# Kernel tuning notes

Measured on AMD Instinct MI355X. Metric: run time of the kernel, lower is better.

Reference implementation:

```python
import jax, jax.numpy as jnp
import numpy as np

H = 200   # hidden_size
P = 4     # maxout_pool_size
T = 4     # max_dec_steps
B = 64
M = 1000
NEG = -1e30


def setup_inputs():
    key = jax.random.key(0)
    ks = jax.random.split(key, 20)
    def rn(k, shape, scale=0.05):
        return jax.random.normal(k, shape, dtype=jnp.float32) * scale
    inp = {}
    inp["U"] = jax.random.normal(ks[0], (B, M, 2 * H), dtype=jnp.float32)
    inp["d_mask"] = jnp.ones((B, M), dtype=jnp.int32)
    inp["span"] = jax.random.randint(ks[1], (B, 2), 0, M)
    # LSTM: input 4H, hidden H, 1 layer, torch forget-gate bias init (f gate = 1)
    inp["w_ih"] = rn(ks[2], (4 * H, 4 * H))
    inp["w_hh"] = rn(ks[3], (4 * H, H))
    inp["b_ih"] = jnp.zeros((4 * H,), jnp.float32).at[H:2 * H].set(1.0)
    inp["b_hh"] = jnp.zeros((4 * H,), jnp.float32)
    # two HighwayMaxout heads (start 's', end 'e')
    for tag, off in (("s", 4), ("e", 11)):
        inp[f"Wr_{tag}"] = rn(ks[off + 0], (H, 5 * H))          # linear, no bias
        inp[f"W1_{tag}"] = rn(ks[off + 1], (H * P, 3 * H))
        inp[f"b1_{tag}"] = jnp.zeros((H * P,), jnp.float32)
        inp[f"W2_{tag}"] = rn(ks[off + 2], (H * P, H))
        inp[f"b2_{tag}"] = jnp.zeros((H * P,), jnp.float32)
        inp[f"W12_{tag}"] = rn(ks[off + 3], (P, 2 * H))
        inp[f"b12_{tag}"] = jnp.zeros((P,), jnp.float32)
    return inp


def lstm_step(x, h, c, w_ih, w_hh, b_ih, b_hh):
    # torch gate order: i, f, g, o
    g = x @ w_ih.T + h @ w_hh.T + b_ih + b_hh
    i, f, gg, o = jnp.split(g, 4, axis=-1)
    c = jax.nn.sigmoid(f) * c + jax.nn.sigmoid(i) * jnp.tanh(gg)
    h = jax.nn.sigmoid(o) * jnp.tanh(c)
    return h, c


def hmn(h, U, u_cat, mask_mult, Wr, W1, b1, W2, b2, W12, b12):
    b, m, _ = U.shape
    r = jnp.tanh(jnp.concatenate([h, u_cat], 1) @ Wr.T)                      # (b,H)
    x = jnp.concatenate([U, jnp.broadcast_to(r[:, None, :], (b, m, H))], 2)  # (b,m,3H)
    m1 = (x @ W1.T + b1).reshape(b, m, H, P).max(-1)                          # (b,m,H)
    m2 = (m1 @ W2.T + b2).reshape(b, m, H, P).max(-1)                         # (b,m,H)
    alpha = (jnp.concatenate([m1, m2], 2) @ W12.T + b12).max(-1)             # (b,m)
    return jax.nn.log_softmax(alpha + mask_mult, axis=1)


def reference(U, d_mask, span, w_ih, w_hh, b_ih, b_hh,
              Wr_s, W1_s, b1_s, W2_s, b2_s, W12_s, b12_s,
              Wr_e, W1_e, b1_e, W2_e, b2_e, W12_e, b12_e):
    b, m, _ = U.shape
    bidx = jnp.arange(b)
    mask_mult = (1.0 - d_mask.astype(jnp.float32)) * NEG
    s_tgt = span[:, 0]
    e_tgt = span[:, 1]
    ps = (Wr_s, W1_s, b1_s, W2_s, b2_s, W12_s, b12_s)
    pe = (Wr_e, W1_e, b1_e, W2_e, b2_e, W12_e, b12_e)

    s0 = jnp.zeros((b,), jnp.int32)
    e0 = (jnp.sum(d_mask, 1) - 1).astype(jnp.int32)
    u_s0 = U[bidx, s0]
    h0 = jnp.zeros((b, H), U.dtype)
    c0 = jnp.zeros((b, H), U.dtype)
    m0 = jnp.ones((b,), bool)

    def step(carry, first):
        s, e, u_s, h, c, ms, me = carry
        u_e = U[bidx, e]
        u_cat = jnp.concatenate([u_s, u_e], 1)               # (b,4H)
        h, c = lstm_step(u_cat, h, c, w_ih, w_hh, b_ih, b_hh)
        # start head
        a_s = hmn(h, U, u_cat, mask_mult, *ps)
        idx_s = jnp.argmax(a_s, 1).astype(jnp.int32)
        s_new = jnp.where(first, idx_s, idx_s * ms)
        ms_new = jnp.where(first, True, s_new != s * ms)
        ls = -jnp.mean(jnp.take_along_axis(a_s, s_tgt[:, None], 1)) * ms_new.astype(U.dtype)
        # end head (u_s refreshed with new start)
        u_s2 = U[bidx, s_new]
        u_cat2 = jnp.concatenate([u_s2, u_e], 1)
        a_e = hmn(h, U, u_cat2, mask_mult, *pe)
        idx_e = jnp.argmax(a_e, 1).astype(jnp.int32)
        e_new = jnp.where(first, idx_e, idx_e * me)
        me_new = jnp.where(first, True, e_new != e * me)
        le = -jnp.mean(jnp.take_along_axis(a_e, e_tgt[:, None], 1)) * me_new.astype(U.dtype)
        return (s_new, e_new, u_s2, h, c, ms_new, me_new), (s_new, ms_new, e_new, me_new, ls + le)

    firsts = jnp.arange(T) == 0
    _, (ss, mss, es, mes, losses) = jax.lax.scan(step, (s0, e0, u_s0, h0, c0, m0, m0), firsts)

    pos_s = jnp.sum(mss.astype(jnp.int32), 0) - 1            # (b,)
    p1 = ss[pos_s, bidx]
    pos_e = jnp.sum(mes.astype(jnp.int32), 0) - 1
    p2 = es[pos_e, bidx]
    loss = jnp.mean(jnp.sum(losses, 0)) / T
    return loss, p1, p2
```

## Files before the change

kernel.cpp:

```cpp
#include <hip/hip_runtime.h>
#include <math.h>

#define H 200
#define TT 4
#define BB 64
#define MM 1000
#define NEGV (-1e30f)

static const int ROWS = BB * MM;
#define KA 416
#define KB 224
#define NPAD 896
#define NSLICE 28
#define LSTR 40
#define RP 500
#define GG 3528

typedef __attribute__((ext_vector_type(8))) short short8;
typedef __attribute__((ext_vector_type(4))) float f32x4;

__device__ __forceinline__ void split2(float x, unsigned short& h, unsigned short& l) {
  unsigned u = __float_as_uint(x);
  h = (unsigned short)(u >> 16);
  float res = x - __uint_as_float(u & 0xffff0000u);
  l = (unsigned short)(__float_as_uint(res) >> 16);
}
__device__ __forceinline__ float bf2f(unsigned short h) {
  return __uint_as_float(((unsigned)h) << 16);
}
__device__ __forceinline__ void gload16(const unsigned short* g, const unsigned short* l) {
  __builtin_amdgcn_global_load_lds(
      (const __attribute__((address_space(1))) void*)g,
      (__attribute__((address_space(3))) void*)l, 16, 0, 0);
}

__global__ __launch_bounds__(256) void k_init(const int* __restrict__ dmask,
    int* st_s, int* st_e, int* ms, int* me,
    float* h, float* c, float* out) {
  int b = blockIdx.x, t = threadIdx.x;
  __shared__ int red[256];
  int sum = 0;
  for (int m = t; m < MM; m += 256) sum += dmask[b * MM + m];
  red[t] = sum; __syncthreads();
  for (int s = 128; s > 0; s >>= 1) { if (t < s) red[t] += red[t + s]; __syncthreads(); }
  if (t == 0) { st_s[b] = 0; st_e[b] = red[0] - 1; ms[b] = 1; me[b] = 1; }
  for (int i = t; i < H; i += 256) { h[b * H + i] = 0.f; c[b * H + i] = 0.f; }
  if (b == 0 && t == 0) out[0] = 0.f;
}

__global__ __launch_bounds__(256) void k_splitP(const float* __restrict__ src, int srcld,
    int Ksrc, int Nsrc,
    unsigned short* __restrict__ hi, unsigned short* __restrict__ lo, int Kpad) {
  int r = blockIdx.x;
  int r7 = r & 127;
  size_t pbase = (size_t)(r >> 7) * (size_t)(128 * Kpad);
  int sw = (r7 >> 1) & 3;
  for (int k = threadIdx.x; k < Kpad; k += 256) {
    unsigned short h = 0, l = 0;
    if (r < Nsrc && k < Ksrc) split2(src[(size_t)r * srcld + k], h, l);
    size_t addr = pbase + (size_t)(k >> 5) * 4096 + r7 * 32 +
                  ((((k >> 3) & 3) ^ sw) << 3) + (k & 7);
    hi[addr] = h; lo[addr] = l;
  }
}

__global__ __launch_bounds__(256) void k_splitPW1(const float* __restrict__ src,
    unsigned short* __restrict__ hi, unsigned short* __restrict__ lo) {
  int r = blockIdx.x;
  int o = (r & ~63) + ((r & 15) << 2) + ((r >> 4) & 3);
  int r7 = r & 127;
  size_t pbase = (size_t)(r >> 7) * (size_t)(128 * KA);
  int sw = (r7 >> 1) & 3;
  for (int k = threadIdx.x; k < KA; k += 256) {
    unsigned short h = 0, l = 0;
    if (o < 800 && k < 400) split2(src[(size_t)o * 600 + k], h, l);
    size_t addr = pbase + (size_t)(k >> 5) * 4096 + r7 * 32 +
                  ((((k >> 3) & 3) ^ sw) << 3) + (k & 7);
    hi[addr] = h; lo[addr] = l;
  }
}

__global__ __launch_bounds__(256) void k_split(const float* __restrict__ src, int srcld,
    int Ksrc, int Nsrc,
    unsigned short* __restrict__ hi, unsigned short* __restrict__ lo, int Kpad) {
  int r = blockIdx.x;
  for (int k = threadIdx.x; k < Kpad; k += 256) {
    unsigned short h = 0, l = 0;
    if (r < Nsrc && k < Ksrc) split2(src[(size_t)r * srcld + k], h, l);
    hi[(size_t)r * Kpad + k] = h;
    lo[(size_t)r * Kpad + k] = l;
  }
}

__global__ __launch_bounds__(1024) void k_lstm_r(
    const float* __restrict__ U, const int* __restrict__ st_s, const int* __restrict__ st_e,
    float* __restrict__ h, float* __restrict__ c,
    const float* __restrict__ w_ih, const float* __restrict__ w_hh,
    const float* __restrict__ b_ih, const float* __restrict__ b_hh,
    const float* __restrict__ Wr, const float* __restrict__ W1, const float* __restrict__ b1,
    float* __restrict__ rcorr, float* __restrict__ ue) {
  int b = blockIdx.x, t = threadIdx.x;
  __shared__ float xc[1000];
  __shared__ float hold[H];
  __shared__ float g[800];
  __shared__ float r[H];
  int si = st_s[b], ei = st_e[b];
  const float* Us = U + ((size_t)b * MM + si) * 400;
  const float* Ue = U + ((size_t)b * MM + ei) * 400;
  if (t < 400) { xc[200 + t] = Us[t]; xc[600 + t] = Ue[t]; ue[b * 400 + t] = Ue[t]; }
  if (t >= 400 && t < 600) hold[t - 400] = h[b * H + (t - 400)];
  __syncthreads();
  if (t < 800) {
    float acc = b_ih[t] + b_hh[t];
    const float4* wi = (const float4*)(w_ih + (size_t)t * 800);
    const float* xv = &xc[200];
    for (int k = 0; k < 200; ++k) {
      float4 wv = wi[k];
      acc = fmaf(wv.x, xv[k * 4 + 0], acc); acc = fmaf(wv.y, xv[k * 4 + 1], acc);
      acc = fmaf(wv.z, xv[k * 4 + 2], acc); acc = fmaf(wv.w, xv[k * 4 + 3], acc);
    }
    const float4* wh = (const float4*)(w_hh + (size_t)t * H);
    for (int k = 0; k < 50; ++k) {
      float4 wv = wh[k];
      acc = fmaf(wv.x, hold[k * 4 + 0], acc); acc = fmaf(wv.y, hold[k * 4 + 1], acc);
      acc = fmaf(wv.z, hold[k * 4 + 2], acc); acc = fmaf(wv.w, hold[k * 4 + 3], acc);
    }
    g[t] = acc;
  }
  __syncthreads();
  if (t < H) {
    float ig = 1.f / (1.f + expf(-g[t]));
    float fg = 1.f / (1.f + expf(-g[H + t]));
    float gg = tanhf(g[2 * H + t]);
    float og = 1.f / (1.f + expf(-g[3 * H + t]));
    float cn = fg * c[b * H + t] + ig * gg;
    c[b * H + t] = cn;
    float hv = og * tanhf(cn);
    h[b * H + t] = hv;
    xc[t] = hv;
  }
  __syncthreads();
  if (t < H) {
    float acc = 0.f;
    const float4* wr = (const float4*)(Wr + (size_t)t * 1000);
    for (int k = 0; k < 250; ++k) {
      float4 wv = wr[k];
      acc = fmaf(wv.x, xc[k * 4 + 0], acc); acc = fmaf(wv.y, xc[k * 4 + 1], acc);
      acc = fmaf(wv.z, xc[k * 4 + 2], acc); acc = fmaf(wv.w, xc[k * 4 + 3], acc);
    }
    r[t] = tanhf(acc);
  }
  __syncthreads();
  if (t < NPAD) {
    float acc = 0.f;
    if (t < 800) {
      acc = b1[t];
      const float4* w1 = (const float4*)(W1 + (size_t)t * 600 + 400);
      for (int k = 0; k < 50; ++k) {
        float4 wv = w1[k];
        acc = fmaf(wv.x, r[k * 4 + 0], acc); acc = fmaf(wv.y, r[k * 4 + 1], acc);
        acc = fmaf(wv.z, r[k * 4 + 2], acc); acc = fmaf(wv.w, r[k * 4 + 3], acc);
      }
    }
    rcorr[b * NPAD + t] = acc;
  }
}

__global__ __launch_bounds__(1024) void k_re(
    const float* __restrict__ U, const int* __restrict__ st_s,
    const float* __restrict__ ue, const float* __restrict__ h,
    const float* __restrict__ Wr, const float* __restrict__ W1, const float* __restrict__ b1,
    float* __restrict__ rcorr) {
  int b = blockIdx.x, t = threadIdx.x;
  __shared__ float xc[1000];
  __shared__ float r[H];
  const float* Us = U + ((size_t)b * MM + st_s[b]) * 400;
  if (t < 200) xc[t] = h[b * H + t];
  if (t >= 200 && t < 600) xc[t] = Us[t - 200];
  if (t >= 600 && t < 1000) xc[t] = ue[b * 400 + (t - 600)];
  __syncthreads();
  if (t < H) {
    float acc = 0.f;
    const float4* wr = (const float4*)(Wr + (size_t)t * 1000);
    for (int k = 0; k < 250; ++k) {
      float4 wv = wr[k];
      acc = fmaf(wv.x, xc[k * 4 + 0], acc); acc = fmaf(wv.y, xc[k * 4 + 1], acc);
      acc = fmaf(wv.z, xc[k * 4 + 2], acc); acc = fmaf(wv.w, xc[k * 4 + 3], acc);
    }
    r[t] = tanhf(acc);
  }
  __syncthreads();
  if (t < NPAD) {
    float acc = 0.f;
    if (t < 800) {
      acc = b1[t];
      const float4* w1 = (const float4*)(W1 + (size_t)t * 600 + 400);
      for (int k = 0; k < 50; ++k) {
        float4 wv = w1[k];
        acc = fmaf(wv.x, r[k * 4 + 0], acc); acc = fmaf(wv.y, r[k * 4 + 1], acc);
        acc = fmaf(wv.z, r[k * 4 + 2], acc); acc = fmaf(wv.w, r[k * 4 + 3], acc);
      }
    }
    rcorr[b * NPAD + t] = acc;
  }
}

template <int MODE>
__global__ __launch_bounds__(256, 3) void k_pgemm(
    const unsigned short* __restrict__ Ah, const unsigned short* __restrict__ Al,
    const unsigned short* __restrict__ Bh, const unsigned short* __restrict__ Bl,
    const float* __restrict__ addv,
    unsigned short* __restrict__ Couth, unsigned short* __restrict__ Coutl,
    float* __restrict__ partial, const float* __restrict__ W12) {
  const int Kpad = (MODE == 0) ? KA : KB;
  const int nk = Kpad >> 5;
  __shared__ unsigned short sA[2][8192];
  __shared__ unsigned short sB[8192];
  const int id = blockIdx.x;
  const int g = id / 56, rem = id % 56;
  const int np = rem >> 3, c8 = rem & 7;
  const int rp = g * 8 + c8;
  if (rp >= RP) return;
  const int tid = threadIdx.x;
  const int lane = tid & 63, wave = tid >> 6;
  const int wm = wave >> 1, wn = wave & 1;
  const int row0 = rp * 128, n0 = np * 128;
  const int lr = lane & 15, ls = lane >> 4;
  const size_t panelA = (size_t)rp * (size_t)(128 * Kpad);
  const size_t panelB = (size_t)np * (size_t)(128 * Kpad);
  const int aoff = (wm * 64 + lr) * 32 + ((ls ^ ((lr >> 1) & 3)) << 3);
  const int boff = (wn * 64 + lr) * 32 + ((ls ^ ((lr >> 1) & 3)) << 3);

  f32x4 acc[4][4];
#pragma unroll
  for (int i = 0; i < 4; ++i)
#pragma unroll
    for (int j = 0; j < 4; ++j) acc[i][j] = (f32x4){0.f, 0.f, 0.f, 0.f};

  auto issueA = [&](int buf, int kt) {
    const size_t tA = panelA + (size_t)kt * 4096;
#pragma unroll
    for (int q = 0; q < 2; ++q) {
      const int cc = (q * 4 + wave) * 512;
      gload16(Ah + tA + cc + lane * 8, &sA[buf][cc]);
      gload16(Al + tA + cc + lane * 8, &sA[buf][4096 + cc]);
    }
  };
  auto issueB = [&](int kt) {
    const size_t tB = panelB + (size_t)kt * 4096;
#pragma unroll
    for (int q = 0; q < 2; ++q) {
      const int cc = (q * 4 + wave) * 512;
      gload16(Bh + tB + cc + lane * 8, &sB[cc]);
      gload16(Bl + tB + cc + lane * 8, &sB[4096 + cc]);
    }
  };

  issueA(0, 0);
  issueB(0);
  int cur = 0;
  for (int kt = 0; kt < nk; ++kt) {
    __syncthreads();
    short8 bh[4], bl[4], fah[4], fal[4];
#pragma unroll
    for (int j = 0; j < 4; ++j) {
      bh[j] = *(const short8*)(sB + boff + j * 512);
      bl[j] = *(const short8*)(sB + 4096 + boff + j * 512);
    }
#pragma unroll
    for (int i = 0; i < 4; ++i) {
      fah[i] = *(const short8*)(&sA[cur][0] + aoff + i * 512);
      fal[i] = *(const short8*)(&sA[cur][0] + 4096 + aoff + i * 512);
    }
    __syncthreads();
    if (kt + 1 < nk) { issueA(cur ^ 1, kt + 1); issueB(kt + 1); }
#pragma unroll
    for (int i = 0; i < 4; ++i)
#pragma unroll
      for (int j = 0; j < 4; ++j)
        acc[i][j] = __builtin_amdgcn_mfma_f32_16x16x32_bf16(fah[i], bh[j], acc[i][j], 0, 0, 0);
#pragma unroll
    for (int i = 0; i < 4; ++i)
#pragma unroll
      for (int j = 0; j < 4; ++j)
        acc[i][j] = __builtin_amdgcn_mfma_f32_16x16x32_bf16(fah[i], bl[j], acc[i][j], 0, 0, 0);
#pragma unroll
    for (int i = 0; i < 4; ++i)
#pragma unroll
      for (int j = 0; j < 4; ++j)
        acc[i][j] = __builtin_amdgcn_mfma_f32_16x16x32_bf16(fal[i], bh[j], acc[i][j], 0, 0, 0);
    cur ^= 1;
  }

  if (MODE == 0) {
    const int obase = n0 + wn * 64 + lr * 4;
    const int po = ((n0 + wn * 64) >> 2) + lr;
    const unsigned b0 = (unsigned)row0 / 1000u;
    const unsigned b1 = (unsigned)(row0 + 127) / 1000u;
    float rc0[4], rc1[4];
#pragma unroll
    for (int j = 0; j < 4; ++j) {
      rc0[j] = addv[b0 * NPAD + obase + j];
      rc1[j] = addv[b1 * NPAD + obase + j];
    }
    const size_t panelC = (size_t)rp * (size_t)(128 * KB);
    const size_t addrBase = panelC + (size_t)(po >> 5) * 4096 + (po & 7);
    const int slotb = (po >> 3) & 3;
    const int rowb7 = wm * 64 + ls * 4;
#pragma unroll
    for (int i = 0; i < 4; ++i) {
#pragma unroll
      for (int r = 0; r < 4; ++r) {
        const int r7 = rowb7 + i * 16 + r;
        const int row = row0 + r7;
        const bool useb0 = ((unsigned)row / 1000u) == b0;
        float v = acc[i][0][r] + (useb0 ? rc0[0] : rc1[0]);
        v = fmaxf(v, acc[i][1][r] + (useb0 ? rc0[1] : rc1[1]));
        v = fmaxf(v, acc[i][2][r] + (useb0 ? rc0[2] : rc1[2]));
        v = fmaxf(v, acc[i][3][r] + (useb0 ? rc0[3] : rc1[3]));
        const int sw = (r7 >> 1) & 3;
        size_t addr = addrBase + r7 * 32 + ((slotb ^ sw) << 3);
        unsigned short hh, ll;
        split2(v, hh, ll);
        Couth[addr] = hh;
        Coutl[addr] = ll;
      }
    }
  } else {
    const int colb = n0 + wn * 64 + lr;
    const int rowb7 = wm * 64 + ls * 4;
    const int pmine = lane & 3;
    float w12j[4], addj[4];
#pragma unroll
    for (int j = 0; j < 4; ++j) {
      const int col = colb + j * 16;
      w12j[j] = (col < 800) ? W12[pmine * 400 + 200 + (col >> 2)] : 0.f;
      addj[j] = (col < 800) ? addv[col] : 0.f;
    }
    const int slice = np * 2 + wn;
#pragma unroll
    for (int i = 0; i < 4; ++i) {
#pragma unroll
      for (int r = 0; r < 4; ++r) {
        const int row = row0 + rowb7 + i * 16 + r;
        float sp = 0.f;
#pragma unroll
        for (int j = 0; j < 4; ++j) {
          float v = acc[i][j][r] + addj[j];
          v = fmaxf(v, __shfl_xor(v, 1));
          v = fmaxf(v, __shfl_xor(v, 2));
          sp = fmaf(v, w12j[j], sp);
        }
        sp += __shfl_xor(sp, 4);
        sp += __shfl_xor(sp, 8);
        if (lr < 4)
          partial[((size_t)row * 14 + slice) * 4 + lr] = sp;
      }
    }
  }
}

__global__ __launch_bounds__(256) void k_m1dot(
    const unsigned short* __restrict__ m1h, const unsigned short* __restrict__ m1l,
    const float* __restrict__ partial, const float* __restrict__ W12,
    const float* __restrict__ b12, float* __restrict__ alpha) {
  __shared__ float w12s[4 * 224];
  __shared__ unsigned short th[4096], tl[4096];
  __shared__ float accs[128 * 8];
  const int t = threadIdx.x;
  const int rp = blockIdx.x;
  for (int i = t; i < 896; i += 256) {
    int p = i / 224, k = i - p * 224;
    w12s[i] = (k < 200) ? W12[p * 400 + k] : 0.f;
  }
  const int r7 = t & 127, hhalf = t >> 7;
  const int sw = (r7 >> 1) & 3;
  float a0 = 0.f, a1 = 0.f, a2 = 0.f, a3 = 0.f;
  const size_t panelC = (size_t)rp * (size_t)(128 * KB);
  for (int kt = 0; kt < 7; ++kt) {
    __syncthreads();
    const size_t tb = panelC + (size_t)kt * 4096;
    *(short8*)&th[t * 16] = *(const short8*)(m1h + tb + t * 16);
    *(short8*)&th[t * 16 + 8] = *(const short8*)(m1h + tb + t * 16 + 8);
    *(short8*)&tl[t * 16] = *(const short8*)(m1l + tb + t * 16);
    *(short8*)&tl[t * 16 + 8] = *(const short8*)(m1l + tb + t * 16 + 8);
    __syncthreads();
#pragma unroll
    for (int cc = 0; cc < 2; ++cc) {
      const int c = hhalf * 2 + cc;
      const short8 hv = *(const short8*)&th[r7 * 32 + ((c ^ sw) << 3)];
      const short8 lv = *(const short8*)&tl[r7 * 32 + ((c ^ sw) << 3)];
      const int kb = kt * 32 + c * 8;
#pragma unroll
      for (int e = 0; e < 8; ++e) {
        float val = bf2f((unsigned short)hv[e]) + bf2f((unsigned short)lv[e]);
        const int k = kb + e;
        a0 = fmaf(val, w12s[0 * 224 + k], a0);
        a1 = fmaf(val, w12s[1 * 224 + k], a1);
        a2 = fmaf(val, w12s[2 * 224 + k], a2);
        a3 = fmaf(val, w12s[3 * 224 + k], a3);
      }
    }
  }
  accs[r7 * 8 + hhalf * 4 + 0] = a0;
  accs[r7 * 8 + hhalf * 4 + 1] = a1;
  accs[r7 * 8 + hhalf * 4 + 2] = a2;
  accs[r7 * 8 + hhalf * 4 + 3] = a3;
  __syncthreads();
  if (t < 128) {
    const size_t row = (size_t)rp * 128 + t;
    float4 bb = *(const float4*)b12;
    float s0 = bb.x + accs[t * 8 + 0] + accs[t * 8 + 4];
    float s1 = bb.y + accs[t * 8 + 1] + accs[t * 8 + 5];
    float s2 = bb.z + accs[t * 8 + 2] + accs[t * 8 + 6];
    float s3 = bb.w + accs[t * 8 + 3] + accs[t * 8 + 7];
    const float4* pr = (const float4*)(partial + row * 56);
#pragma unroll
    for (int s = 0; s < 14; ++s) {
      float4 p4 = pr[s];
      s0 += p4.x; s1 += p4.y; s2 += p4.z; s3 += p4.w;
    }
    alpha[row] = fmaxf(fmaxf(s0, s1), fmaxf(s2, s3));
  }
}

__global__ __launch_bounds__(256) void k_argmax(const float* __restrict__ alpha,
    const int* __restrict__ dmask, const int* __restrict__ span, int tag,
    int* __restrict__ idx_out, float* __restrict__ atgt_out) {
  int b = blockIdx.x, t = threadIdx.x;
  __shared__ float vals[MM];
  __shared__ float rv[256];
  __shared__ int ri[256];
  float bestv = -3.4e38f; int besti = 0x7fffffff;
  for (int m = t; m < MM; m += 256) {
    float v = alpha[b * MM + m];
    if (!dmask[b * MM + m]) v += NEGV;
    vals[m] = v;
    if (v > bestv || (v == bestv && m < besti)) { bestv = v; besti = m; }
  }
  rv[t] = bestv; ri[t] = besti; __syncthreads();
  for (int s = 128; s > 0; s >>= 1) {
    if (t < s) {
      float v2 = rv[t + s]; int i2 = ri[t + s];
      if (v2 > rv[t] || (v2 == rv[t] && i2 < ri[t])) { rv[t] = v2; ri[t] = i2; }
    }
    __syncthreads();
  }
  float vmax = rv[0]; int vidx = ri[0];
  __syncthreads();
  float se = 0.f;
  for (int m = t; m < MM; m += 256) se += expf(vals[m] - vmax);
  rv[t] = se; __syncthreads();
  for (int s = 128; s > 0; s >>= 1) { if (t < s) rv[t] += rv[t + s]; __syncthreads(); }
  if (t == 0) {
    int tgt = span[b * 2 + tag];
    atgt_out[b] = vals[tgt] - vmax - logf(rv[0]);
    idx_out[b] = vidx;
  }
}

template <int MODE, int PRESPLIT>
__global__ __launch_bounds__(256) void k_mgemm(
    const float* __restrict__ Af, int lda, int KsrcA,
    const unsigned short* __restrict__ Ah, const unsigned short* __restrict__ Al,
    const unsigned short* __restrict__ Bh, const unsigned short* __restrict__ Bl, int Kpad,
    const float* __restrict__ addv,
    unsigned short* __restrict__ Couth, unsigned short* __restrict__ Coutl,
    float* __restrict__ partial, const float* __restrict__ W12, int slice_base) {
  __shared__ unsigned short sAh[128 * LSTR], sAl[128 * LSTR];
  __shared__ unsigned short sBh[128 * LSTR], sBl[128 * LSTR];
  const int tid = threadIdx.x;
  const int lane = tid & 63, wave = tid >> 6;
  const int wm = wave >> 1, wn = wave & 1;
  const int n0 = blockIdx.x * 128, row0 = blockIdx.y * 128;
  const int lr = lane & 15, ls = lane >> 4;
  f32x4 acc[4][4];
#pragma unroll
  for (int i = 0; i < 4; ++i)
#pragma unroll
    for (int j = 0; j < 4; ++j) acc[i][j] = (f32x4){0.f, 0.f, 0.f, 0.f};
  const int srow = tid >> 1, shalf = tid & 1;
  const float* Afp = Af ? (Af + (size_t)(row0 + srow) * lda + shalf * 16) : nullptr;
  const unsigned short* Ahp = Ah ? (Ah + (size_t)(row0 + srow) * Kpad + shalf * 16) : nullptr;
  const unsigned short* Alp = Al ? (Al + (size_t)(row0 + srow) * Kpad + shalf * 16) : nullptr;
  const unsigned short* Bhp = Bh + (size_t)(n0 + srow) * Kpad + shalf * 16;
  const unsigned short* Blp = Bl + (size_t)(n0 + srow) * Kpad + shalf * 16;
  const int wo = srow * LSTR + shalf * 16;
  const int aoff = (wm * 64 + lr) * LSTR + ls * 8;
  const int boff = (wn * 64 + lr) * LSTR + ls * 8;
  short8 rah0, rah1, ral0, ral1, rbh0, rbh1, rbl0, rbl1;
  auto loadk = [&](int kt) {
    if (PRESPLIT) {
      rah0 = *(const short8*)(Ahp + kt * 32);
      rah1 = *(const short8*)(Ahp + kt * 32 + 8);
      ral0 = *(const short8*)(Alp + kt * 32);
      ral1 = *(const short8*)(Alp + kt * 32 + 8);
    } else {
      const int kk = kt * 32 + shalf * 16;
      float av[16];
#pragma unroll
      for (int q = 0; q < 4; ++q) {
        float4 v;
        if (kk + q * 4 + 4 <= KsrcA) v = *(const float4*)(Afp + kt * 32 + q * 4);
        else v = make_float4(0.f, 0.f, 0.f, 0.f);
        av[q * 4 + 0] = v.x; av[q * 4 + 1] = v.y;
        av[q * 4 + 2] = v.z; av[q * 4 + 3] = v.w;
      }
#pragma unroll
      for (int e = 0; e < 8; ++e) {
        unsigned short hh, ll;
        split2(av[e], hh, ll);     rah0[e] = (short)hh; ral0[e] = (short)ll;
        split2(av[8 + e], hh, ll); rah1[e] = (short)hh; ral1[e] = (short)ll;
      }
    }
    rbh0 = *(const short8*)(Bhp + kt * 32);
    rbh1 = *(const short8*)(Bhp + kt * 32 + 8);
    rbl0 = *(const short8*)(Blp + kt * 32);
    rbl1 = *(const short8*)(Blp + kt * 32 + 8);
  };
  const int nk = Kpad >> 5;
  loadk(0);
  for (int kt = 0; kt < nk; ++kt) {
    *(short8*)&sAh[wo] = rah0; *(short8*)&sAh[wo + 8] = rah1;
    *(short8*)&sAl[wo] = ral0; *(short8*)&sAl[wo + 8] = ral1;
    *(short8*)&sBh[wo] = rbh0; *(short8*)&sBh[wo + 8] = rbh1;
    *(short8*)&sBl[wo] = rbl0; *(short8*)&sBl[wo + 8] = rbl1;
    __syncthreads();
    if (kt + 1 < nk) loadk(kt + 1);
    short8 fa[4], fb[4];
#pragma unroll
    for (int i = 0; i < 4; ++i) fa[i] = *(const short8*)&sAh[aoff + i * 16 * LSTR];
#pragma unroll
    for (int j = 0; j < 4; ++j) fb[j] = *(const short8*)&sBh[boff + j * 16 * LSTR];
#pragma unroll
    for (int i = 0; i < 4; ++i)
#pragma unroll
      for (int j = 0; j < 4; ++j)
        acc[i][j] = __builtin_amdgcn_mfma_f32_16x16x32_bf16(fa[i], fb[j], acc[i][j], 0, 0, 0);
    short8 fc[4];
#pragma unroll
    for (int j = 0; j < 4; ++j) fc[j] = *(const short8*)&sBl[boff + j * 16 * LSTR];
#pragma unroll
    for (int i = 0; i < 4; ++i)
#pragma unroll
      for (int j = 0; j < 4; ++j)
        acc[i][j] = __builtin_amdgcn_mfma_f32_16x16x32_bf16(fa[i], fc[j], acc[i][j], 0, 0, 0);
#pragma unroll
    for (int i = 0; i < 4; ++i) fa[i] = *(const short8*)&sAl[aoff + i * 16 * LSTR];
#pragma unroll
    for (int i = 0; i < 4; ++i)
#pragma unroll
      for (int j = 0; j < 4; ++j)
        acc[i][j] = __builtin_amdgcn_mfma_f32_16x16x32_bf16(fa[i], fb[j], acc[i][j], 0, 0, 0);
    __syncthreads();
  }
  const int colb = n0 + wn * 64 + lr;
  const int rowb = row0 + wm * 64 + ls * 4;
  const int pmine = lane & 3;
  const int woff = (MODE == 0) ? 0 : 200;
  float w12j[4], addj[4];
#pragma unroll
  for (int j = 0; j < 4; ++j) {
    const int col = colb + j * 16;
    w12j[j] = (col < 800) ? W12[pmine * 400 + woff + (col >> 2)] : 0.f;
    if (MODE == 1) addj[j] = (col < 800) ? addv[col] : 0.f;
  }
  const int slice = slice_base + blockIdx.x * 2 + wn;
#pragma unroll
  for (int i = 0; i < 4; ++i) {
#pragma unroll
    for (int r = 0; r < 4; ++r) {
      const int row = rowb + i * 16 + r;
      float sp = 0.f;
#pragma unroll
      for (int j = 0; j < 4; ++j) {
        const int col = colb + j * 16;
        float v = acc[i][j][r];
        if (MODE == 0) {
          const unsigned bidx = (unsigned)row / 1000u;
          v += addv[bidx * NPAD + col];
        } else {
          v += addj[j];
        }
        v = fmaxf(v, __shfl_xor(v, 1));
        v = fmaxf(v, __shfl_xor(v, 2));
        if (MODE == 0 && (lane & 3) == 0) {
          unsigned short hh, ll;
          split2(v, hh, ll);
          Couth[(size_t)row * KB + (col >> 2)] = hh;
          Coutl[(size_t)row * KB + (col >> 2)] = ll;
        }
        sp = fmaf(v, w12j[j], sp);
      }
      sp += __shfl_xor(sp, 4);
      sp += __shfl_xor(sp, 8);
      if (lr < 4)
        partial[((size_t)row * NSLICE + slice) * 4 + lr] = sp;
    }
  }
}

__global__ __launch_bounds__(256) void k_reduce(const float* __restrict__ partial,
    const float* __restrict__ b12, const int* __restrict__ dmask,
    const int* __restrict__ span, int tag,
    int* __restrict__ idx_out, float* __restrict__ atgt_out) {
  int b = blockIdx.x, t = threadIdx.x;
  __shared__ float vals[MM];
  __shared__ float rv[256];
  __shared__ int ri[256];
  float4 bb = *(const float4*)b12;
  float bestv = -3.4e38f; int besti = 0x7fffffff;
  for (int m = t; m < MM; m += 256) {
    const float4* pr = (const float4*)(partial + ((size_t)(b * MM + m)) * (NSLICE * 4));
    float4 a4 = bb;
#pragma unroll
    for (int s = 0; s < NSLICE; ++s) {
      float4 p4 = pr[s];
      a4.x += p4.x; a4.y += p4.y; a4.z += p4.z; a4.w += p4.w;
    }
    float v = fmaxf(fmaxf(a4.x, a4.y), fmaxf(a4.z, a4.w));
    if (!dmask[b * MM + m]) v += NEGV;
    vals[m] = v;
    if (v > bestv || (v == bestv && m < besti)) { bestv = v; besti = m; }
  }
  rv[t] = bestv; ri[t] = besti; __syncthreads();
  for (int s = 128; s > 0; s >>= 1) {
    if (t < s) {
      float v2 = rv[t + s]; int i2 = ri[t + s];
      if (v2 > rv[t] || (v2 == rv[t] && i2 < ri[t])) { rv[t] = v2; ri[t] = i2; }
    }
    __syncthreads();
  }
  float vmax = rv[0]; int vidx = ri[0];
  __syncthreads();
  float se = 0.f;
  for (int m = t; m < MM; m += 256) se += expf(vals[m] - vmax);
  rv[t] = se; __syncthreads();
  for (int s = 128; s > 0; s >>= 1) { if (t < s) rv[t] += rv[t + s]; __syncthreads(); }
  if (t == 0) {
    int tgt = span[b * 2 + tag];
    atgt_out[b] = vals[tgt] - vmax - logf(rv[0]);
    idx_out[b] = vidx;
  }
}

__global__ __launch_bounds__(64) void k_update(const int* __restrict__ idx_buf,
    const float* __restrict__ atgt, int* __restrict__ st, int* __restrict__ mstate,
    float* __restrict__ pout, float* __restrict__ loss, int first) {
  int b = threadIdx.x;
  int idx = idx_buf[b];
  int sold = st[b], msold = mstate[b];
  int snew = first ? idx : (msold ? idx : 0);
  int msnew = first ? 1 : ((snew != (msold ? sold : 0)) ? 1 : 0);
  st[b] = snew; mstate[b] = msnew;
  if (msnew) pout[b] = (float)snew;
  float asum = atgt[b];
  float csum = (float)msnew;
  for (int off = 32; off > 0; off >>= 1) {
    asum += __shfl_down(asum, off);
    csum += __shfl_down(csum, off);
  }
  if (b == 0) loss[0] += (-asum / (float)BB) * csum / (float)(BB * TT);
}

extern "C" void kernel_launch(void* const* d_in, const int* in_sizes, int n_in,
                              void* d_out, int out_size, void* d_ws, size_t ws_size,
                              hipStream_t stream) {
  const float* U     = (const float*)d_in[0];
  const int*   dmask = (const int*)d_in[1];
  const int*   span  = (const int*)d_in[2];
  const float* w_ih  = (const float*)d_in[3];
  const float* w_hh  = (const float*)d_in[4];
  const float* b_ih  = (const float*)d_in[5];
  const float* b_hh  = (const float*)d_in[6];
  const float* Wr[2]  = {(const float*)d_in[7],  (const float*)d_in[14]};
  const float* W1[2]  = {(const float*)d_in[8],  (const float*)d_in[15]};
  const float* b1[2]  = {(const float*)d_in[9],  (const float*)d_in[16]};
  const float* W2[2]  = {(const float*)d_in[10], (const float*)d_in[17]};
  const float* b2[2]  = {(const float*)d_in[11], (const float*)d_in[18]};
  const float* W12[2] = {(const float*)d_in[12], (const float*)d_in[19]};
  const float* b12[2] = {(const float*)d_in[13], (const float*)d_in[20]};
  float* out = (float*)d_out;

  size_t off = 0;
  char* base = (char*)d_ws;
  auto alloc = [&](size_t n) {
    void* p = base + off;
    off += (n + 255) & ~(size_t)255;
    return p;
  };
  unsigned short* m1h = (unsigned short*)alloc((size_t)ROWS * KB * 2);
  unsigned short* m1l = (unsigned short*)alloc((size_t)ROWS * KB * 2);
  float* partial = (float*)alloc((size_t)ROWS * NSLICE * 4 * 4);
  float* alphab  = (float*)alloc((size_t)ROWS * 4);
  float* rcorr   = (float*)alloc((size_t)BB * NPAD * 4);
  float* ue      = (float*)alloc((size_t)BB * 400 * 4);
  float* hbuf    = (float*)alloc((size_t)BB * H * 4);
  float* cbuf    = (float*)alloc((size_t)BB * H * 4);
  float* atgt    = (float*)alloc((size_t)BB * 4);
  int* st_s = (int*)alloc(BB * 4);
  int* st_e = (int*)alloc(BB * 4);
  int* msb  = (int*)alloc(BB * 4);
  int* meb  = (int*)alloc(BB * 4);
  int* idxb = (int*)alloc(BB * 4);
  unsigned short *W1h[2], *W1l[2], *W2h[2], *W2l[2];
  for (int g = 0; g < 2; ++g) {
    W1h[g] = (unsigned short*)alloc((size_t)NPAD * KA * 2);
    W1l[g] = (unsigned short*)alloc((size_t)NPAD * KA * 2);
    W2h[g] = (unsigned short*)alloc((size_t)NPAD * KB * 2);
    W2l[g] = (unsigned short*)alloc((size_t)NPAD * KB * 2);
  }
  const size_t UHL_B = (size_t)ROWS * KA * 2;
  bool panelPath = (ws_size >= off + 2 * UHL_B + 4096);
  unsigned short *Uh = nullptr, *Ul = nullptr;
  if (panelPath) {
    Uh = (unsigned short*)alloc(UHL_B);
    Ul = (unsigned short*)alloc(UHL_B);
  }

  k_init<<<BB, 256, 0, stream>>>(dmask, st_s, st_e, msb, meb, hbuf, cbuf, out);
  if (panelPath) {
    for (int g = 0; g < 2; ++g) {
      k_splitPW1<<<NPAD, 256, 0, stream>>>(W1[g], W1h[g], W1l[g]);
      k_splitP<<<NPAD, 256, 0, stream>>>(W2[g], 200, 200, 800, W2h[g], W2l[g], KB);
    }
    k_splitP<<<ROWS, 256, 0, stream>>>(U, 400, 400, ROWS, Uh, Ul, KA);

    for (int t = 0; t < TT; ++t) {
      int first = (t == 0) ? 1 : 0;
      for (int tag = 0; tag < 2; ++tag) {
        if (tag == 0)
          k_lstm_r<<<BB, 1024, 0, stream>>>(U, st_s, st_e, hbuf, cbuf, w_ih, w_hh, b_ih, b_hh,
                                            Wr[0], W1[0], b1[0], rcorr, ue);
        else
          k_re<<<BB, 1024, 0, stream>>>(U, st_s, ue, hbuf, Wr[1], W1[1], b1[1], rcorr);

        k_pgemm<0><<<GG, 256, 0, stream>>>(Uh, Ul, W1h[tag], W1l[tag],
            rcorr, m1h, m1l, nullptr, nullptr);
        k_pgemm<1><<<GG, 256, 0, stream>>>(m1h, m1l, W2h[tag], W2l[tag],
            b2[tag], nullptr, nullptr, partial, W12[tag]);
        k_m1dot<<<RP, 256, 0, stream>>>(m1h, m1l, partial, W12[tag], b12[tag], alphab);
        k_argmax<<<BB, 256, 0, stream>>>(alphab, dmask, span, tag, idxb, atgt);

        if (tag == 0)
          k_update<<<1, 64, 0, stream>>>(idxb, atgt, st_s, msb, out + 1, out, first);
        else
          k_update<<<1, 64, 0, stream>>>(idxb, atgt, st_e, meb, out + 1 + BB, out, first);
      }
    }
  } else {
    for (int g = 0; g < 2; ++g) {
      k_split<<<NPAD, 256, 0, stream>>>(W1[g], 600, 400, 800, W1h[g], W1l[g], KA);
      k_split<<<NPAD, 256, 0, stream>>>(W2[g], 200, 200, 800, W2h[g], W2l[g], KB);
    }
    dim3 gg(NPAD / 128, ROWS / 128);
    for (int t = 0; t < TT; ++t) {
      int first = (t == 0) ? 1 : 0;
      for (int tag = 0; tag < 2; ++tag) {
        if (tag == 0)
          k_lstm_r<<<BB, 1024, 0, stream>>>(U, st_s, st_e, hbuf, cbuf, w_ih, w_hh, b_ih, b_hh,
                                            Wr[0], W1[0], b1[0], rcorr, ue);
        else
          k_re<<<BB, 1024, 0, stream>>>(U, st_s, ue, hbuf, Wr[1], W1[1], b1[1], rcorr);

        k_mgemm<0, 0><<<gg, 256, 0, stream>>>(U, 400, 400, nullptr, nullptr,
            W1h[tag], W1l[tag], KA, rcorr, m1h, m1l, partial, W12[tag], 0);
        k_mgemm<1, 1><<<gg, 256, 0, stream>>>(nullptr, 0, 0, m1h, m1l,
            W2h[tag], W2l[tag], KB, b2[tag], nullptr, nullptr, partial, W12[tag], 14);

        k_reduce<<<BB, 256, 0, stream>>>(partial, b12[tag], dmask, span, tag, idxb, atgt);
        if (tag == 0)
          k_update<<<1, 64, 0, stream>>>(idxb, atgt, st_s, msb, out + 1, out, first);
        else
          k_update<<<1, 64, 0, stream>>>(idxb, atgt, st_e, meb, out + 1 + BB, out, first);
      }
    }
  }
}
```

Baseline: 2.438 ms.

## Split per-batch LSTM and reduction kernels into multi-block transposed-weight matvecs

Replaces the single 1024-thread-per-batch LSTM/r/rcorr kernels with a chain of small kernels (prep, gates, activation, r, rcorr). Each is gridded over output tiles and batch and reads pre-transposed weights, so loads are coalesced and more CUs are used. Weight transposes run once up front. The partial buffer is shrunk to 14 slices on the panel path. The cost is more kernel launches per step and extra workspace, and the panel path now needs a larger workspace to be selected.

```diff
diff --git a/kernel.cpp b/kernel.cpp
--- a/kernel.cpp
+++ b/kernel.cpp
@@ -46,6 +46,13 @@
   if (t == 0) { st_s[b] = 0; st_e[b] = red[0] - 1; ms[b] = 1; me[b] = 1; }
   for (int i = t; i < H; i += 256) { h[b * H + i] = 0.f; c[b * H + i] = 0.f; }
   if (b == 0 && t == 0) out[0] = 0.f;
+}
+
+__global__ __launch_bounds__(256) void k_T(const float* __restrict__ src, int ld,
+    int R, int koff, float* __restrict__ dst) {
+  int k = blockIdx.x;
+  for (int r = threadIdx.x; r < R; r += 256)
+    dst[(size_t)k * R + r] = src[(size_t)r * ld + koff + k];
 }
 
 __global__ __launch_bounds__(256) void k_splitP(const float* __restrict__ src, int srcld,
@@ -90,6 +97,110 @@
     hi[(size_t)r * Kpad + k] = h;
     lo[(size_t)r * Kpad + k] = l;
   }
+}
+
+__global__ __launch_bounds__(256) void k_prep(const float* __restrict__ U,
+    const int* __restrict__ st_s, const int* __restrict__ st_e,
+    float* __restrict__ ucat, float* __restrict__ ue) {
+  int b = blockIdx.x, t = threadIdx.x;
+  int si = st_s[b], ei = st_e[b];
+  const float* Us = U + ((size_t)b * MM + si) * 400;
+  const float* Ue = U + ((size_t)b * MM + ei) * 400;
+  for (int i = t; i < 400; i += 256) {
+    float uv = Ue[i];
+    ucat[b * 800 + i] = Us[i];
+    ucat[b * 800 + 400 + i] = uv;
+    ue[b * 400 + i] = uv;
+  }
+}
+
+__global__ __launch_bounds__(256) void k_gates(
+    const float* __restrict__ ucat, const float* __restrict__ hbuf,
+    const float* __restrict__ wTih, const float* __restrict__ wThh,
+    const float* __restrict__ b_ih, const float* __restrict__ b_hh,
+    float* __restrict__ g) {
+  const int b = blockIdx.y, t = threadIdx.x;
+  const int o = blockIdx.x * 64 + (t & 63);
+  const int oc = o < 800 ? o : 799;
+  const int ks = t >> 6;
+  __shared__ float xs[800], hs[200], red[256];
+  for (int i = t; i < 800; i += 256) xs[i] = ucat[b * 800 + i];
+  for (int i = t; i < 200; i += 256) hs[i] = hbuf[b * H + i];
+  __syncthreads();
+  float acc = 0.f;
+#pragma unroll 8
+  for (int k = ks * 200; k < ks * 200 + 200; ++k)
+    acc = fmaf(wTih[(size_t)k * 800 + oc], xs[k], acc);
+#pragma unroll 8
+  for (int k = ks * 50; k < ks * 50 + 50; ++k)
+    acc = fmaf(wThh[(size_t)k * 800 + oc], hs[k], acc);
+  red[t] = acc; __syncthreads();
+  if (ks == 0 && o < 800)
+    g[b * 800 + o] = red[t] + red[t + 64] + red[t + 128] + red[t + 192] + b_ih[o] + b_hh[o];
+}
+
+__global__ __launch_bounds__(256) void k_act(const float* __restrict__ g,
+    float* __restrict__ h, float* __restrict__ c) {
+  int b = blockIdx.x, t = threadIdx.x;
+  if (t >= H) return;
+  float ig = 1.f / (1.f + expf(-g[b * 800 + t]));
+  float fg = 1.f / (1.f + expf(-g[b * 800 + 200 + t]));
+  float gg = tanhf(g[b * 800 + 400 + t]);
+  float og = 1.f / (1.f + expf(-g[b * 800 + 600 + t]));
+  float cn = fg * c[b * H + t] + ig * gg;
+  c[b * H + t] = cn;
+  h[b * H + t] = og * tanhf(cn);
+}
+
+template <int TAG>
+__global__ __launch_bounds__(256) void k_r2(
+    const float* __restrict__ U, const int* __restrict__ st_s,
+    const float* __restrict__ ucat, const float* __restrict__ ue,
+    const float* __restrict__ hbuf, const float* __restrict__ WrT,
+    float* __restrict__ rbuf) {
+  const int b = blockIdx.y, t = threadIdx.x;
+  const int o = blockIdx.x * 64 + (t & 63);
+  const int oc = o < 200 ? o : 199;
+  const int ks = t >> 6;
+  __shared__ float xcs[1000], red[256];
+  for (int i = t; i < 200; i += 256) xcs[i] = hbuf[b * H + i];
+  if (TAG == 0) {
+    for (int i = t; i < 800; i += 256) xcs[200 + i] = ucat[b * 800 + i];
+  } else {
+    const float* Us = U + ((size_t)b * MM + st_s[b]) * 400;
+    for (int i = t; i < 400; i += 256) {
+      xcs[200 + i] = Us[i];
+      xcs[600 + i] = ue[b * 400 + i];
+    }
+  }
+  __syncthreads();
+  float acc = 0.f;
+#pragma unroll 8
+  for (int k = ks * 250; k < ks * 250 + 250; ++k)
+    acc = fmaf(WrT[(size_t)k * 200 + oc], xcs[k], acc);
+  red[t] = acc; __syncthreads();
+  if (ks == 0 && o < 200)
+    rbuf[b * 200 + o] = tanhf(red[t] + red[t + 64] + red[t + 128] + red[t + 192]);
+}
+
+__global__ __launch_bounds__(256) void k_rcorr(
+    const float* __restrict__ rbuf, const float* __restrict__ W1cT,
+    const float* __restrict__ b1, float* __restrict__ rcorr) {
+  const int b = blockIdx.y, t = threadIdx.x;
+  const int o = blockIdx.x * 64 + (t & 63);
+  const int oc = o < 800 ? o : 799;
+  const int ks = t >> 6;
+  __shared__ float rs[200], red[256];
+  for (int i = t; i < 200; i += 256) rs[i] = rbuf[b * 200 + i];
+  __syncthreads();
+  float acc = 0.f;
+#pragma unroll 8
+  for (int k = ks * 50; k < ks * 50 + 50; ++k)
+    acc = fmaf(W1cT[(size_t)k * 800 + oc], rs[k], acc);
+  red[t] = acc; __syncthreads();
+  if (ks == 0)
+    rcorr[b * NPAD + o] = (o < 800)
+        ? red[t] + red[t + 64] + red[t + 128] + red[t + 192] + b1[o] : 0.f;
 }
 
 __global__ __launch_bounds__(1024) void k_lstm_r(
@@ -689,15 +800,15 @@
     off += (n + 255) & ~(size_t)255;
     return p;
   };
-  unsigned short* m1h = (unsigned short*)alloc((size_t)ROWS * KB * 2);
-  unsigned short* m1l = (unsigned short*)alloc((size_t)ROWS * KB * 2);
-  float* partial = (float*)alloc((size_t)ROWS * NSLICE * 4 * 4);
-  float* alphab  = (float*)alloc((size_t)ROWS * 4);
-  float* rcorr   = (float*)alloc((size_t)BB * NPAD * 4);
-  float* ue      = (float*)alloc((size_t)BB * 400 * 4);
-  float* hbuf    = (float*)alloc((size_t)BB * H * 4);
-  float* cbuf    = (float*)alloc((size_t)BB * H * 4);
-  float* atgt    = (float*)alloc((size_t)BB * 4);
+  float* rcorr = (float*)alloc((size_t)BB * NPAD * 4);
+  float* ue    = (float*)alloc((size_t)BB * 400 * 4);
+  float* ucat  = (float*)alloc((size_t)BB * 800 * 4);
+  float* gbuf  = (float*)alloc((size_t)BB * 800 * 4);
+  float* rbuf  = (float*)alloc((size_t)BB * 200 * 4);
+  float* hbuf  = (float*)alloc((size_t)BB * H * 4);
+  float* cbuf  = (float*)alloc((size_t)BB * H * 4);
+  float* alphab = (float*)alloc((size_t)ROWS * 4);
+  float* atgt  = (float*)alloc((size_t)BB * 4);
   int* st_s = (int*)alloc(BB * 4);
   int* st_e = (int*)alloc(BB * 4);
   int* msb  = (int*)alloc(BB * 4);
@@ -710,45 +821,66 @@
     W2h[g] = (unsigned short*)alloc((size_t)NPAD * KB * 2);
     W2l[g] = (unsigned short*)alloc((size_t)NPAD * KB * 2);
   }
-  const size_t UHL_B = (size_t)ROWS * KA * 2;
-  bool panelPath = (ws_size >= off + 2 * UHL_B + 4096);
-  unsigned short *Uh = nullptr, *Ul = nullptr;
+  unsigned short* m1h = (unsigned short*)alloc((size_t)ROWS * KB * 2);
+  unsigned short* m1l = (unsigned short*)alloc((size_t)ROWS * KB * 2);
+
+  const size_t P14_B  = (size_t)ROWS * 14 * 4 * 4;
+  const size_t TIH_B  = (size_t)800 * 800 * 4;
+  const size_t THH_B  = (size_t)200 * 800 * 4;
+  const size_t TWR_B  = (size_t)1000 * 200 * 4;
+  const size_t TW1_B  = (size_t)200 * 800 * 4;
+  const size_t UHL_B  = (size_t)ROWS * KA * 2;
+  size_t panel_need = off + P14_B + TIH_B + THH_B + 2 * TWR_B + 2 * TW1_B + 2 * UHL_B + 4096;
+  bool panelPath = (ws_size >= panel_need);
+
   if (panelPath) {
-    Uh = (unsigned short*)alloc(UHL_B);
-    Ul = (unsigned short*)alloc(UHL_B);
-  }
-
-  k_init<<<BB, 256, 0, stream>>>(dmask, st_s, st_e, msb, meb, hbuf, cbuf, out);
-  if (panelPath) {
+    float* partial = (float*)alloc(P14_B);
+    float* wTih = (float*)alloc(TIH_B);
+    float* wThh = (float*)alloc(THH_B);
+    float* WrT[2]  = {(float*)alloc(TWR_B), (float*)alloc(TWR_B)};
+    float* W1cT[2] = {(float*)alloc(TW1_B), (float*)alloc(TW1_B)};
+    unsigned short* Uh = (unsigned short*)alloc(UHL_B);
+    unsigned short* Ul = (unsigned short*)alloc(UHL_B);
+
+    k_init<<<BB, 256, 0, stream>>>(dmask, st_s, st_e, msb, meb, hbuf, cbuf, out);
     for (int g = 0; g < 2; ++g) {
       k_splitPW1<<<NPAD, 256, 0, stream>>>(W1[g], W1h[g], W1l[g]);
       k_splitP<<<NPAD, 256, 0, stream>>>(W2[g], 200, 200, 800, W2h[g], W2l[g], KB);
-    }
+      k_T<<<1000, 256, 0, stream>>>(Wr[g], 1000, 200, 0, WrT[g]);
+      k_T<<<200, 256, 0, stream>>>(W1[g], 600, 800, 400, W1cT[g]);
+    }
+    k_T<<<800, 256, 0, stream>>>(w_ih, 800, 800, 0, wTih);
+    k_T<<<200, 256, 0, stream>>>(w_hh, 200, 800, 0, wThh);
     k_splitP<<<ROWS, 256, 0, stream>>>(U, 400, 400, ROWS, Uh, Ul, KA);
 
+    dim3 g13(13, BB), g4(4, BB), g14(14, BB);
     for (int t = 0; t < TT; ++t) {
       int first = (t == 0) ? 1 : 0;
-      for (int tag = 0; tag < 2; ++tag) {
-        if (tag == 0)
-          k_lstm_r<<<BB, 1024, 0, stream>>>(U, st_s, st_e, hbuf, cbuf, w_ih, w_hh, b_ih, b_hh,
-                                            Wr[0], W1[0], b1[0], rcorr, ue);
-        else
-          k_re<<<BB, 1024, 0, stream>>>(U, st_s, ue, hbuf, Wr[1], W1[1], b1[1], rcorr);
-
-        k_pgemm<0><<<GG, 256, 0, stream>>>(Uh, Ul, W1h[tag], W1l[tag],
-            rcorr, m1h, m1l, nullptr, nullptr);
-        k_pgemm<1><<<GG, 256, 0, stream>>>(m1h, m1l, W2h[tag], W2l[tag],
-            b2[tag], nullptr, nullptr, partial, W12[tag]);
-        k_m1dot<<<RP, 256, 0, stream>>>(m1h, m1l, partial, W12[tag], b12[tag], alphab);
-        k_argmax<<<BB, 256, 0, stream>>>(alphab, dmask, span, tag, idxb, atgt);
-
-        if (tag == 0)
-          k_update<<<1, 64, 0, stream>>>(idxb, atgt, st_s, msb, out + 1, out, first);
-        else
-          k_update<<<1, 64, 0, stream>>>(idxb, atgt, st_e, meb, out + 1 + BB, out, first);
-      }
+      k_prep<<<BB, 256, 0, stream>>>(U, st_s, st_e, ucat, ue);
+      k_gates<<<g13, 256, 0, stream>>>(ucat, hbuf, wTih, wThh, b_ih, b_hh, gbuf);
+      k_act<<<BB, 256, 0, stream>>>(gbuf, hbuf, cbuf);
+      k_r2<0><<<g4, 256, 0, stream>>>(U, st_s, ucat, ue, hbuf, WrT[0], rbuf);
+      k_rcorr<<<g14, 256, 0, stream>>>(rbuf, W1cT[0], b1[0], rcorr);
+      k_pgemm<0><<<GG, 256, 0, stream>>>(Uh, Ul, W1h[0], W1l[0],
+          rcorr, m1h, m1l, nullptr, nullptr);
+      k_pgemm<1><<<GG, 256, 0, stream>>>(m1h, m1l, W2h[0], W2l[0],
+          b2[0], nullptr, nullptr, partial, W12[0]);
+      k_m1dot<<<RP, 256, 0, stream>>>(m1h, m1l, partial, W12[0], b12[0], alphab);
+      k_argmax<<<BB, 256, 0, stream>>>(alphab, dmask, span, 0, idxb, atgt);
+      k_update<<<1, 64, 0, stream>>>(idxb, atgt, st_s, msb, out + 1, out, first);
+      k_r2<1><<<g4, 256, 0, stream>>>(U, st_s, ucat, ue, hbuf, WrT[1], rbuf);
+      k_rcorr<<<g14, 256, 0, stream>>>(rbuf, W1cT[1], b1[1], rcorr);
+      k_pgemm<0><<<GG, 256, 0, stream>>>(Uh, Ul, W1h[1], W1l[1],
+          rcorr, m1h, m1l, nullptr, nullptr);
+      k_pgemm<1><<<GG, 256, 0, stream>>>(m1h, m1l, W2h[1], W2l[1],
+          b2[1], nullptr, nullptr, partial, W12[1]);
+      k_m1dot<<<RP, 256, 0, stream>>>(m1h, m1l, partial, W12[1], b12[1], alphab);
+      k_argmax<<<BB, 256, 0, stream>>>(alphab, dmask, span, 1, idxb, atgt);
+      k_update<<<1, 64, 0, stream>>>(idxb, atgt, st_e, meb, out + 1 + BB, out, first);
     }
   } else {
+    float* partial = (float*)alloc((size_t)ROWS * NSLICE * 4 * 4);
+    k_init<<<BB, 256, 0, stream>>>(dmask, st_s, st_e, msb, meb, hbuf, cbuf, out);
     for (int g = 0; g < 2; ++g) {
       k_split<<<NPAD, 256, 0, stream>>>(W1[g], 600, 400, 800, W1h[g], W1l[g], KA);
       k_split<<<NPAD, 256, 0, stream>>>(W2[g], 200, 200, 800, W2h[g], W2l[g], KB);
```

Result: faster. 2.063 ms (-15.4%).
